# Kernel tuning notes

Hardware: AMD Instinct MI355X
Metric: run time of the kernel (lower is better)

## Reference

```python
import jax, jax.numpy as jnp
import numpy as np
from jax import lax

B, S, T, V, E, H = 32, 128, 64, 32000, 512, 512
STEPS = T - 1


def gru_cell(x, h, Wih, Whh, bih, bhh):
    # PyTorch GRU cell: gates ordered (r, z, n)
    gi = x @ Wih.T + bih            # [B, 3H]
    gh = h @ Whh.T + bhh            # [B, 3H]
    ir, iz, inn = jnp.split(gi, 3, axis=-1)
    hr, hz, hn = jnp.split(gh, 3, axis=-1)
    r = jax.nn.sigmoid(ir + hr)
    z = jax.nn.sigmoid(iz + hz)
    n = jnp.tanh(inn + r * hn)
    return (1.0 - z) * n + z * h


def setup_inputs() -> dict:
    key = jax.random.key(0)
    ks = jax.random.split(key, 16)
    w = lambda k, shape: (jax.random.normal(k, shape, dtype=jnp.float32) * 0.05)
    src = jax.random.randint(ks[0], (B, S), 1, V)
    src_lengths = jax.random.randint(ks[1], (B,), 1, S + 1)
    tgt = jax.random.randint(ks[2], (B, T), 1, V)
    return {
        'src': src, 'src_lengths': src_lengths, 'tgt': tgt,
        # encoder
        'emb_enc': w(ks[3], (V, E)).at[0].set(0.0),   # padding_idx=0
        'Wih_e': w(ks[4], (3 * H, E)),
        'Whh_e': w(ks[5], (3 * H, H)),
        'bih_e': jnp.zeros((3 * H,), jnp.float32),
        'bhh_e': jnp.zeros((3 * H,), jnp.float32),
        # decoder
        'emb_dec': w(ks[6], (V, E)).at[0].set(0.0),
        'Wih_d': w(ks[7], (3 * H, E + H)),
        'Whh_d': w(ks[8], (3 * H, H)),
        'bih_d': jnp.zeros((3 * H,), jnp.float32),
        'bhh_d': jnp.zeros((3 * H,), jnp.float32),
        'Wc': w(ks[9], (H, 2 * H)),
        'bc': jnp.zeros((H,), jnp.float32),
        'Wo': w(ks[10], (V, H)),
        'bo': jnp.zeros((V,), jnp.float32),
    }


def _forward(src, src_lengths, tgt, emb_enc, Wih_e, Whh_e, bih_e, bhh_e,
             emb_dec, Wih_d, Whh_d, bih_d, bhh_d, Wc, bc, Wo, bo):
    # ---- encoder (packed-sequence semantics: state frozen / outputs zero past length) ----
    x = emb_enc[src]                                   # [B, S, E]
    xs = jnp.swapaxes(x, 0, 1)                         # [S, B, E]
    valid = jnp.arange(S)[:, None] < src_lengths[None, :]  # [S, B]
    h0 = jnp.zeros((src.shape[0], H), x.dtype)

    def enc_step(h, inp):
        xt, vt = inp
        hn = gru_cell(xt, h, Wih_e, Whh_e, bih_e, bhh_e)
        h = jnp.where(vt[:, None], hn, h)
        out = jnp.where(vt[:, None], hn, 0.0)
        return h, out

    h_enc, enc_outs = lax.scan(enc_step, h0, (xs, valid))
    enc_outs = jnp.swapaxes(enc_outs, 0, 1)            # [B, S, H]
    mask = jnp.arange(S)[None, :] < src_lengths[:, None]  # [B, S]

    # ---- decoder loop (teacher forcing ratio 1.0 -> input = tgt[:, t]) ----
    tokens = jnp.swapaxes(tgt[:, :STEPS], 0, 1)        # [STEPS, B]

    def dec_step(h, tok):
        e = emb_dec[tok]                               # [B, E]
        query = h                                      # hidden[-1], 1 layer
        scores = jnp.einsum('bsh,bh->bs', enc_outs, query)
        scores = jnp.where(mask, scores, -jnp.inf)
        aw = jax.nn.softmax(scores, axis=1)            # [B, S]
        ctx = jnp.einsum('bs,bsh->bh', aw, enc_outs)   # [B, H]
        rnn_in = jnp.concatenate([e, ctx], axis=-1)    # [B, E+H]
        hn = gru_cell(rnn_in, h, Wih_d, Whh_d, bih_d, bhh_d)
        cc = jnp.tanh(jnp.concatenate([hn, ctx], axis=-1) @ Wc.T + bc)
        logits = cc @ Wo.T + bo                        # [B, V]
        return hn, (logits, aw)

    _, (logits, attns) = lax.scan(dec_step, h_enc, tokens)
    logits = jnp.swapaxes(logits, 0, 1)                # [B, STEPS, V]
    attns = jnp.swapaxes(attns, 0, 1)                  # [B, STEPS, S]
    return logits, attns


def reference(src, src_lengths, tgt, emb_enc, Wih_e, Whh_e, bih_e, bhh_e,
              emb_dec, Wih_d, Whh_d, bih_d, bhh_d, Wc, bc, Wo, bo):
    return _forward(src, src_lengths, tgt, emb_enc, Wih_e, Whh_e, bih_e, bhh_e,
                    emb_dec, Wih_d, Whh_d, bih_d, bhh_d, Wc, bc, Wo, bo)
```

## Files before the change

### kernel.cpp

```cpp
#include <hip/hip_runtime.h>
#include <hip/hip_fp16.h>
#include <cmath>

#define B_ 32
#define S_ 128
#define T_ 64
#define STEPS_ 63
#define V_ 32000
#define E_ 512
#define H_ 512

typedef __attribute__((ext_vector_type(4))) float f32x4;
typedef __attribute__((ext_vector_type(8))) short bf16x8;
typedef __attribute__((ext_vector_type(2))) _Float16 f16x2;

__device__ inline short f2bf(float x) {
  unsigned u = __builtin_bit_cast(unsigned, x);
  u = (u + 0x7fffu + ((u >> 16) & 1u)) >> 16;
  return (short)u;
}
__device__ inline float bf2f(short h) {
  unsigned u = ((unsigned)(unsigned short)h) << 16;
  return __builtin_bit_cast(float, u);
}
__device__ inline float fdot2(__half2 a, __half2 b, float c) {
#if __has_builtin(__builtin_amdgcn_fdot2)
  return __builtin_amdgcn_fdot2(__builtin_bit_cast(f16x2, a),
                                __builtin_bit_cast(f16x2, b), c, false);
#else
  float2 af = __half22float2(a), bf = __half22float2(b);
  return c + af.x * bf.x + af.y * bf.y;
#endif
}
__device__ inline __half2 bc2(unsigned v) { return __builtin_bit_cast(__half2, v); }
__device__ inline float sigm(float x) { return 1.f / (1.f + expf(-x)); }

__global__ __launch_bounds__(256) void k_pack_w3(
    const float* __restrict__ W, int ldw, int col0, __half* __restrict__ W3) {
  int idx = blockIdx.x * 256 + threadIdx.x;
  int up = idx & 255, g = (idx >> 8) % 3, kq = idx / 768;
  const float* r0 = W + (long)(g * 512 + 2 * up) * ldw + col0 + 4 * kq;
  const float* r1 = r0 + ldw;
  __half h[8];
  h[0] = __float2half(r0[0]); h[1] = __float2half(r0[1]);
  h[2] = __float2half(r1[0]); h[3] = __float2half(r1[1]);
  h[4] = __float2half(r0[2]); h[5] = __float2half(r0[3]);
  h[6] = __float2half(r1[2]); h[7] = __float2half(r1[3]);
  *(uint4*)(W3 + (long)idx * 8) = *(uint4*)h;
}

__global__ __launch_bounds__(256) void k_mfma_gemm(
    const float* __restrict__ A, const float* __restrict__ emb,
    const int* __restrict__ tok, int amode,
    const float* __restrict__ Bmat, long ldb,
    const float* __restrict__ bias,
    void* __restrict__ outp, long sb, long st,
    int M, int N, int K, int outmode, int passes) {
  __shared__ short Ah[128 * 40];
  __shared__ short Al[128 * 40];
  __shared__ short Bh[128 * 40];
  __shared__ short Bl[128 * 40];
  int t = threadIdx.x;
  int n0 = blockIdx.x * 128, m0 = blockIdx.y * 128;
  int ar = t >> 2, ac = (t & 3) * 8;

  const float* arow0;
  const float* arow1;
  {
    int m = m0 + ar;       int mc = m < M ? m : M - 1;
    int m2 = m0 + ar + 64; int mc2 = m2 < M ? m2 : M - 1;
    if (amode == 0) {
      arow0 = A + (long)mc * K;
      arow1 = A + (long)mc2 * K;
    } else {
      int b = mc & 31, q = mc >> 5;
      int tk = (amode == 1) ? tok[b * S_ + q] : tok[b * T_ + q];
      arow0 = emb + (long)tk * K;
      b = mc2 & 31; q = mc2 >> 5;
      tk = (amode == 1) ? tok[b * S_ + q] : tok[b * T_ + q];
      arow1 = emb + (long)tk * K;
    }
  }
  const float* brow0 = Bmat + (long)(n0 + ar) * ldb;
  const float* brow1 = Bmat + (long)(n0 + ar + 64) * ldb;

  int lane = t & 63, wave = t >> 6;
  int wm = (wave >> 1) * 64, wn = (wave & 1) * 64;
  int lr = lane & 15, lk = lane >> 4;
  f32x4 acc[4][4] = {};

  for (int k0 = 0; k0 < K; k0 += 32) {
    auto stage = [&](const float* rowp, short* Dh, short* Dl, int r) {
      float4 x0 = *(const float4*)(rowp + k0 + ac);
      float4 x1 = *(const float4*)(rowp + k0 + ac + 4);
      float xs[8] = {x0.x, x0.y, x0.z, x0.w, x1.x, x1.y, x1.z, x1.w};
      bf16x8 hi, lo;
#pragma unroll
      for (int i = 0; i < 8; ++i) {
        short h = f2bf(xs[i]);
        hi[i] = h;
        lo[i] = f2bf(xs[i] - bf2f(h));
      }
      *(bf16x8*)&Dh[r * 40 + ac] = hi;
      if (passes > 1) *(bf16x8*)&Dl[r * 40 + ac] = lo;
    };
    stage(arow0, Ah, Al, ar);
    stage(arow1, Ah, Al, ar + 64);
    stage(brow0, Bh, Bl, ar);
    stage(brow1, Bh, Bl, ar + 64);
    __syncthreads();

    bf16x8 a_h[4], b_h[4];
#pragma unroll
    for (int i = 0; i < 4; ++i) {
      a_h[i] = *(const bf16x8*)&Ah[(wm + i * 16 + lr) * 40 + lk * 8];
      b_h[i] = *(const bf16x8*)&Bh[(wn + i * 16 + lr) * 40 + lk * 8];
    }
    if (passes > 1) {
      bf16x8 a_l[4], b_l[4];
#pragma unroll
      for (int i = 0; i < 4; ++i) {
        a_l[i] = *(const bf16x8*)&Al[(wm + i * 16 + lr) * 40 + lk * 8];
        b_l[i] = *(const bf16x8*)&Bl[(wn + i * 16 + lr) * 40 + lk * 8];
      }
#pragma unroll
      for (int i = 0; i < 4; ++i)
#pragma unroll
        for (int j = 0; j < 4; ++j) {
          acc[i][j] = __builtin_amdgcn_mfma_f32_16x16x32_bf16(a_l[i], b_h[j], acc[i][j], 0, 0, 0);
          acc[i][j] = __builtin_amdgcn_mfma_f32_16x16x32_bf16(a_h[i], b_l[j], acc[i][j], 0, 0, 0);
        }
    }
#pragma unroll
    for (int i = 0; i < 4; ++i)
#pragma unroll
      for (int j = 0; j < 4; ++j)
        acc[i][j] = __builtin_amdgcn_mfma_f32_16x16x32_bf16(a_h[i], b_h[j], acc[i][j], 0, 0, 0);
    __syncthreads();
  }

#pragma unroll
  for (int i = 0; i < 4; ++i) {
#pragma unroll
    for (int r = 0; r < 4; ++r) {
      int m = m0 + wm + i * 16 + lk * 4 + r;
      if (m >= M) continue;
      long base = (long)(m & 31) * sb + (long)(m >> 5) * st;
#pragma unroll
      for (int j = 0; j < 4; ++j) {
        int n = n0 + wn + j * 16 + lr;
        float v = acc[i][j][r] + bias[n];
        if (outmode == 2) ((__half*)outp)[base + n] = __float2half(v);
        else ((float*)outp)[base + n] = (outmode == 1) ? tanhf(v) : v;
      }
    }
  }
}

__global__ __launch_bounds__(1024) void k_enc_all(
    const float* __restrict__ gi_all,
    const __half* __restrict__ W3,
    const float* __restrict__ bhh, const int* __restrict__ lens,
    float* __restrict__ h_out,
    __half* __restrict__ EO16,
    float* __restrict__ EO32) {
  __shared__ __align__(8) __half2 hs16[256];
  __shared__ float pGh[1536];
  __shared__ float gis[1536];
  int b = blockIdx.x, t = threadIdx.x;
  int len = lens[b];
  float br0 = 0, br1 = 0, bz0 = 0, bz1 = 0, bn0 = 0, bn1 = 0, hold0 = 0, hold1 = 0;
  if (t < 256) {
    br0 = bhh[2 * t]; br1 = bhh[2 * t + 1];
    bz0 = bhh[512 + 2 * t]; bz1 = bhh[512 + 2 * t + 1];
    bn0 = bhh[1024 + 2 * t]; bn1 = bhh[1024 + 2 * t + 1];
    hs16[t] = __float22half2_rn(make_float2(0.f, 0.f));
  }
  __syncthreads();

  for (int s = 0; s < S_; ++s) {
    if (s == len) break;
    if (t >= 256) {
      int c = t - 256, g = c >> 8, up = c & 255;
      const __half* wb = W3 + (long)(g * 256 + up) * 8;
      float a0 = 0.f, a1 = 0.f;
#pragma unroll 8
      for (int kq = 0; kq < 128; ++kq) {
        uint4 w8 = *(const uint4*)(wb + (long)kq * 6144);
        __half2 x01 = hs16[2 * kq], x23 = hs16[2 * kq + 1];
        a0 = fdot2(x01, bc2(w8.x), a0); a1 = fdot2(x01, bc2(w8.y), a1);
        a0 = fdot2(x23, bc2(w8.z), a0); a1 = fdot2(x23, bc2(w8.w), a1);
      }
      pGh[g * 512 + 2 * up] = a0;
      pGh[g * 512 + 2 * up + 1] = a1;
    } else {
      const float* gi = gi_all + ((long)s * 32 + b) * 1536;
      int i0 = t * 6;
#pragma unroll
      for (int i = 0; i < 6; ++i) gis[i0 + i] = gi[i0 + i];
    }
    __syncthreads();
    if (t < 256) {
      int u0 = 2 * t;
      float r0 = sigm(gis[u0] + pGh[u0] + br0);
      float r1 = sigm(gis[u0 + 1] + pGh[u0 + 1] + br1);
      float z0 = sigm(gis[512 + u0] + pGh[512 + u0] + bz0);
      float z1 = sigm(gis[512 + u0 + 1] + pGh[512 + u0 + 1] + bz1);
      float n0 = tanhf(gis[1024 + u0] + r0 * (pGh[1024 + u0] + bn0));
      float n1 = tanhf(gis[1024 + u0 + 1] + r1 * (pGh[1024 + u0 + 1] + bn1));
      hold0 = (1.f - z0) * n0 + z0 * hold0;
      hold1 = (1.f - z1) * n1 + z1 * hold1;
      __half2 h2 = __float22half2_rn(make_float2(hold0, hold1));
      hs16[t] = h2;
      long row = (long)b * 128 + s;
      *(__half2*)(EO16 + row * 512 + u0) = h2;
      *(float2*)(EO32 + row * 512 + u0) = make_float2(hold0, hold1);
    }
    __syncthreads();
  }
  if (t < 256) *(float2*)(h_out + b * 512 + 2 * t) = make_float2(hold0, hold1);
}

__global__ __launch_bounds__(1024) void k_dec_all(
    const float* __restrict__ gie,
    const __half* __restrict__ EO16g,
    const __half* __restrict__ W3,
    const __half* __restrict__ GV,
    const float* __restrict__ bhh, const int* __restrict__ lens,
    const float* __restrict__ h_init,
    float* __restrict__ hctx,
    float* __restrict__ attns) {
  __shared__ __align__(16) __half2 EOs[32768];
  __shared__ __align__(8) __half2 hs16[256];
  __shared__ float pGh[1536];
  __shared__ float pGc[1536];
  __shared__ float gis[1536];
  __shared__ float sc[128];
  int b = blockIdx.x, t = threadIdx.x;
  int lane = t & 63, wave = t >> 6;
  int len = lens[b];
  float br0 = 0, br1 = 0, bz0 = 0, bz1 = 0, bn0 = 0, bn1 = 0, hold0 = 0, hold1 = 0;
  if (t < 256) {
    br0 = bhh[2 * t]; br1 = bhh[2 * t + 1];
    bz0 = bhh[512 + 2 * t]; bz1 = bhh[512 + 2 * t + 1];
    bn0 = bhh[1024 + 2 * t]; bn1 = bhh[1024 + 2 * t + 1];
    float2 h2 = *(const float2*)(h_init + b * 512 + 2 * t);
    hold0 = h2.x; hold1 = h2.y;
    hs16[t] = __float22half2_rn(h2);
  }
  {
    const uint4* src = (const uint4*)(EO16g + (long)b * 128 * 512);
    uint4* dst = (uint4*)EOs;
    for (int i = t; i < 8192; i += 1024) dst[i] = src[i];
  }
  __syncthreads();
  const __half2* GVb = (const __half2*)GV + (long)b * 128 * 768;

  for (int step = 0; step < STEPS_; ++step) {
    long row = (long)step * 32 + b;
    if (t < 768) {
      int g = t >> 8, up = t & 255;
      const __half* wb = W3 + (long)(g * 256 + up) * 8;
      float a0 = 0.f, a1 = 0.f;
#pragma unroll 8
      for (int kq = 0; kq < 128; ++kq) {
        uint4 w8 = *(const uint4*)(wb + (long)kq * 6144);
        __half2 x01 = hs16[2 * kq], x23 = hs16[2 * kq + 1];
        a0 = fdot2(x01, bc2(w8.x), a0); a1 = fdot2(x01, bc2(w8.y), a1);
        a0 = fdot2(x23, bc2(w8.z), a0); a1 = fdot2(x23, bc2(w8.w), a1);
      }
      pGh[g * 512 + 2 * up] = a0;
      pGh[g * 512 + 2 * up + 1] = a1;
    } else {
      int w = wave - 12;
      uint4 hv = ((const uint4*)hs16)[lane];
      __half2 h0 = bc2(hv.x), h1 = bc2(hv.y), h2 = bc2(hv.z), h3 = bc2(hv.w);
#pragma unroll 4
      for (int si = 0; si < 32; ++si) {
        int s = w * 32 + si;
        uint4 ev = ((const uint4*)&EOs[s * 256])[lane];
        float p = 0.f;
        p = fdot2(bc2(ev.x), h0, p);
        p = fdot2(bc2(ev.y), h1, p);
        p = fdot2(bc2(ev.z), h2, p);
        p = fdot2(bc2(ev.w), h3, p);
#pragma unroll
        for (int off = 32; off > 0; off >>= 1) p += __shfl_down(p, off, 64);
        if (lane == 0) sc[s] = p;
      }
    }
    __syncthreads();
    if (t < 64) {
      float p0 = sc[lane], p1 = sc[64 + lane];
      bool v0 = lane < len, v1 = 64 + lane < len;
      float m = fmaxf(v0 ? p0 : -INFINITY, v1 ? p1 : -INFINITY);
#pragma unroll
      for (int off = 32; off > 0; off >>= 1) m = fmaxf(m, __shfl_xor(m, off, 64));
      float e0 = v0 ? expf(p0 - m) : 0.f;
      float e1 = v1 ? expf(p1 - m) : 0.f;
      float S = e0 + e1;
#pragma unroll
      for (int off = 32; off > 0; off >>= 1) S += __shfl_xor(S, off, 64);
      float aw0 = e0 / S, aw1 = e1 / S;
      sc[lane] = aw0;
      sc[64 + lane] = aw1;
      float* ap = attns + ((long)b * STEPS_ + step) * 128;
      ap[lane] = aw0;
      ap[64 + lane] = aw1;
    } else if (t < 448) {
      int i0 = (t - 64) * 4;
      *(float4*)(gis + i0) = *(const float4*)(gie + row * 1536 + i0);
    }
    __syncthreads();
    if (t < 768) {
      float ax = 0.f, ay = 0.f;
      for (int s = 0; s < 128; ++s) {
        if (s == len) break;
        float aw = sc[s];
        float2 g2 = __half22float2(GVb[(long)s * 768 + t]);
        ax += aw * g2.x;
        ay += aw * g2.y;
      }
      pGc[2 * t] = ax;
      pGc[2 * t + 1] = ay;
    } else {
      int c = t - 768;
      float ax = 0.f, ay = 0.f;
      for (int s = 0; s < 128; ++s) {
        if (s == len) break;
        float aw = sc[s];
        float2 e2 = __half22float2(EOs[s * 256 + c]);
        ax += aw * e2.x;
        ay += aw * e2.y;
      }
      *(float2*)(hctx + row * 1024 + 512 + 2 * c) = make_float2(ax, ay);
    }
    __syncthreads();
    if (t < 256) {
      int u0 = 2 * t;
      float r0 = sigm(gis[u0] + pGc[u0] + pGh[u0] + br0);
      float r1 = sigm(gis[u0 + 1] + pGc[u0 + 1] + pGh[u0 + 1] + br1);
      float z0 = sigm(gis[512 + u0] + pGc[512 + u0] + pGh[512 + u0] + bz0);
      float z1 = sigm(gis[512 + u0 + 1] + pGc[512 + u0 + 1] + pGh[512 + u0 + 1] + bz1);
      float n0 = tanhf(gis[1024 + u0] + pGc[1024 + u0] + r0 * (pGh[1024 + u0] + bn0));
      float n1 = tanhf(gis[1024 + u0 + 1] + pGc[1024 + u0 + 1] + r1 * (pGh[1024 + u0 + 1] + bn1));
      hold0 = (1.f - z0) * n0 + z0 * hold0;
      hold1 = (1.f - z1) * n1 + z1 * hold1;
      hs16[t] = __float22half2_rn(make_float2(hold0, hold1));
      *(float2*)(hctx + row * 1024 + u0) = make_float2(hold0, hold1);
    }
    __syncthreads();
  }
}

extern "C" void kernel_launch(void* const* d_in, const int* in_sizes, int n_in,
                              void* d_out, int out_size, void* d_ws, size_t ws_size,
                              hipStream_t stream) {
  (void)in_sizes; (void)n_in; (void)out_size; (void)ws_size;
  const int*   src   = (const int*)d_in[0];
  const int*   lens  = (const int*)d_in[1];
  const int*   tgt   = (const int*)d_in[2];
  const float* emb_e = (const float*)d_in[3];
  const float* Wih_e = (const float*)d_in[4];
  const float* Whh_e = (const float*)d_in[5];
  const float* bih_e = (const float*)d_in[6];
  const float* bhh_e = (const float*)d_in[7];
  const float* emb_d = (const float*)d_in[8];
  const float* Wih_d = (const float*)d_in[9];
  const float* Whh_d = (const float*)d_in[10];
  const float* bih_d = (const float*)d_in[11];
  const float* bhh_d = (const float*)d_in[12];
  const float* Wc    = (const float*)d_in[13];
  const float* bc    = (const float*)d_in[14];
  const float* Wo    = (const float*)d_in[15];
  const float* bo    = (const float*)d_in[16];

  float* logits = (float*)d_out;
  float* attns  = (float*)d_out + (long)B_ * STEPS_ * V_;

  float* w = (float*)d_ws;
  __half* W3e  = (__half*)w;
  __half* W3d  = (__half*)(w + 393216);
  float*  zb   = w + 786432;
  float*  GIe  = w + 788480;
  float*  GId  = GIe + 6291456;
  __half* EO16 = (__half*)(GId + 3145728);
  float*  EO32 = GId + 3145728 + 1048576;
  float*  h0   = EO32 + 2097152;
  __half* GV    = (__half*)GIe;
  float*  hctx  = GIe + 3145728;
  float*  ccall = GIe + 5242880;

  hipMemsetAsync(EO16, 0, 2097152 * sizeof(__half), stream);
  hipMemsetAsync(EO32, 0, 2097152 * sizeof(float), stream);
  hipMemsetAsync(zb, 0, 1536 * sizeof(float), stream);

  k_pack_w3<<<384, 256, 0, stream>>>(Whh_e, 512, 0, W3e);
  k_pack_w3<<<384, 256, 0, stream>>>(Whh_d, 512, 0, W3d);

  k_mfma_gemm<<<dim3(1536 / 128, 4096 / 128), 256, 0, stream>>>(
      nullptr, emb_e, src, 1, Wih_e, 512, bih_e, GIe, 1536L, 32L * 1536L,
      4096, 1536, 512, 0, 1);
  k_mfma_gemm<<<dim3(1536 / 128, (2016 + 127) / 128), 256, 0, stream>>>(
      nullptr, emb_d, tgt, 2, Wih_d, 1024, bih_d, GId, 1536L, 32L * 1536L,
      2016, 1536, 512, 0, 1);

  k_enc_all<<<32, 1024, 0, stream>>>(GIe, W3e, bhh_e, lens, h0, EO16, EO32);

  k_mfma_gemm<<<dim3(1536 / 128, 4096 / 128), 256, 0, stream>>>(
      EO32, nullptr, nullptr, 0, Wih_d + 512, 1024, zb, GV, 1536L, 49152L,
      4096, 1536, 512, 2, 1);

  k_dec_all<<<32, 1024, 0, stream>>>(GId, EO16, W3d, GV, bhh_d, lens, h0,
                                     hctx, attns);

  k_mfma_gemm<<<dim3(512 / 128, (2016 + 127) / 128), 256, 0, stream>>>(
      hctx, nullptr, nullptr, 0, Wc, 1024, bc, ccall, 512L, 16384L,
      2016, 512, 1024, 1, 1);

  k_mfma_gemm<<<dim3(V_ / 128, (2016 + 127) / 128), 256, 0, stream>>>(
      ccall, nullptr, nullptr, 0, Wo, 512, bo, logits,
      (long)STEPS_ * V_, (long)V_, 2016, 32000, 512, 0, 1);
}
```

Measured before the change: 2.976 ms.

## Split encoder GRU recurrence across two cooperating blocks per batch with flag sync

Each batch row's encoder recurrence is now handled by two blocks, each computing half the hidden units and half of each K reduction per thread. The halves exchange fp16 hidden state through a global buffer and release/acquire flags every timestep. The aim is to halve the per-step serial matvec latency and use more CUs. In exchange it adds cross-block spin-wait latency each step and relies on all 64 blocks being co-resident.

Result: slower. 3.162 ms (+6.3%).

```diff
diff --git a/kernel.cpp b/kernel.cpp
--- a/kernel.cpp
+++ b/kernel.cpp
@@ -163,62 +163,103 @@
     const float* __restrict__ bhh, const int* __restrict__ lens,
     float* __restrict__ h_out,
     __half* __restrict__ EO16,
-    float* __restrict__ EO32) {
+    float* __restrict__ EO32,
+    unsigned* __restrict__ hbuf,
+    int* __restrict__ flags) {
   __shared__ __align__(8) __half2 hs16[256];
-  __shared__ float pGh[1536];
-  __shared__ float gis[1536];
-  int b = blockIdx.x, t = threadIdx.x;
+  __shared__ float pGh[768];
+  __shared__ float gis[768];
+  int blk = blockIdx.x, t = threadIdx.x;
+  int b = blk & 31, half = blk >> 5;
   int len = lens[b];
-  float br0 = 0, br1 = 0, bz0 = 0, bz1 = 0, bn0 = 0, bn1 = 0, hold0 = 0, hold1 = 0;
-  if (t < 256) {
-    br0 = bhh[2 * t]; br1 = bhh[2 * t + 1];
-    bz0 = bhh[512 + 2 * t]; bz1 = bhh[512 + 2 * t + 1];
-    bn0 = bhh[1024 + 2 * t]; bn1 = bhh[1024 + 2 * t + 1];
-    hs16[t] = __float22half2_rn(make_float2(0.f, 0.f));
-  }
+  int u0g = half * 256;
+  int* flagOwn = flags + b * 2 + half;
+  int* flagP   = flags + b * 2 + (1 - half);
+  unsigned* hbOwn = hbuf + (b * 2 + half) * 128;
+  unsigned* hbP   = hbuf + (b * 2 + (1 - half)) * 128;
+  float br0 = 0, br1 = 0, bz0 = 0, bz1 = 0, bn0 = 0, bn1 = 0;
+  float hold0 = 0.f, hold1 = 0.f;
+  if (t < 128) {
+    int u = u0g + 2 * t;
+    br0 = bhh[u]; br1 = bhh[u + 1];
+    bz0 = bhh[512 + u]; bz1 = bhh[512 + u + 1];
+    bn0 = bhh[1024 + u]; bn1 = bhh[1024 + u + 1];
+  }
+  if (t < 256) hs16[t] = __float22half2_rn(make_float2(0.f, 0.f));
   __syncthreads();
+
+  int c = t - 256;
+  int g = c >> 8, rem = c & 255;
+  int up_loc = rem >> 1, kh2 = rem & 1;
+  int up = half * 128 + up_loc;
+  const __half* wb = W3 + (long)(kh2 * 64) * 6144 + (long)(g * 256 + up) * 8;
 
   for (int s = 0; s < S_; ++s) {
     if (s == len) break;
+    if (s > 0) {
+      if (t == 0) {
+        while (__hip_atomic_load(flagP, __ATOMIC_ACQUIRE, __HIP_MEMORY_SCOPE_AGENT) < s)
+          __builtin_amdgcn_s_sleep(1);
+      }
+      __syncthreads();
+      if (t < 128) {
+        unsigned v = __hip_atomic_load(hbP + t, __ATOMIC_RELAXED, __HIP_MEMORY_SCOPE_AGENT);
+        hs16[(1 - half) * 128 + t] = bc2(v);
+      }
+    }
+    __syncthreads();
     if (t >= 256) {
-      int c = t - 256, g = c >> 8, up = c & 255;
-      const __half* wb = W3 + (long)(g * 256 + up) * 8;
       float a0 = 0.f, a1 = 0.f;
 #pragma unroll 8
-      for (int kq = 0; kq < 128; ++kq) {
-        uint4 w8 = *(const uint4*)(wb + (long)kq * 6144);
+      for (int kq2 = 0; kq2 < 64; ++kq2) {
+        uint4 w8 = *(const uint4*)(wb + (long)kq2 * 6144);
+        int kq = kh2 * 64 + kq2;
         __half2 x01 = hs16[2 * kq], x23 = hs16[2 * kq + 1];
         a0 = fdot2(x01, bc2(w8.x), a0); a1 = fdot2(x01, bc2(w8.y), a1);
         a0 = fdot2(x23, bc2(w8.z), a0); a1 = fdot2(x23, bc2(w8.w), a1);
       }
-      pGh[g * 512 + 2 * up] = a0;
-      pGh[g * 512 + 2 * up + 1] = a1;
-    } else {
+      a0 += __shfl_xor(a0, 1, 64);
+      a1 += __shfl_xor(a1, 1, 64);
+      if (kh2 == 0) {
+        pGh[g * 256 + 2 * up_loc] = a0;
+        pGh[g * 256 + 2 * up_loc + 1] = a1;
+      }
+    } else if (t >= 128) {
       const float* gi = gi_all + ((long)s * 32 + b) * 1536;
-      int i0 = t * 6;
-#pragma unroll
-      for (int i = 0; i < 6; ++i) gis[i0 + i] = gi[i0 + i];
-    }
-    __syncthreads();
-    if (t < 256) {
-      int u0 = 2 * t;
-      float r0 = sigm(gis[u0] + pGh[u0] + br0);
-      float r1 = sigm(gis[u0 + 1] + pGh[u0 + 1] + br1);
-      float z0 = sigm(gis[512 + u0] + pGh[512 + u0] + bz0);
-      float z1 = sigm(gis[512 + u0 + 1] + pGh[512 + u0 + 1] + bz1);
-      float n0 = tanhf(gis[1024 + u0] + r0 * (pGh[1024 + u0] + bn0));
-      float n1 = tanhf(gis[1024 + u0 + 1] + r1 * (pGh[1024 + u0 + 1] + bn1));
+      int i = t - 128;
+      gis[2 * i] = gi[u0g + 2 * i];
+      gis[2 * i + 1] = gi[u0g + 2 * i + 1];
+      gis[256 + 2 * i] = gi[512 + u0g + 2 * i];
+      gis[256 + 2 * i + 1] = gi[512 + u0g + 2 * i + 1];
+      gis[512 + 2 * i] = gi[1024 + u0g + 2 * i];
+      gis[512 + 2 * i + 1] = gi[1024 + u0g + 2 * i + 1];
+    }
+    __syncthreads();
+    if (t < 128) {
+      int l0 = 2 * t;
+      float r0 = sigm(gis[l0] + pGh[l0] + br0);
+      float r1 = sigm(gis[l0 + 1] + pGh[l0 + 1] + br1);
+      float z0 = sigm(gis[256 + l0] + pGh[256 + l0] + bz0);
+      float z1 = sigm(gis[256 + l0 + 1] + pGh[256 + l0 + 1] + bz1);
+      float n0 = tanhf(gis[512 + l0] + r0 * (pGh[512 + l0] + bn0));
+      float n1 = tanhf(gis[512 + l0 + 1] + r1 * (pGh[512 + l0 + 1] + bn1));
       hold0 = (1.f - z0) * n0 + z0 * hold0;
       hold1 = (1.f - z1) * n1 + z1 * hold1;
       __half2 h2 = __float22half2_rn(make_float2(hold0, hold1));
-      hs16[t] = h2;
+      hs16[half * 128 + t] = h2;
       long row = (long)b * 128 + s;
-      *(__half2*)(EO16 + row * 512 + u0) = h2;
-      *(float2*)(EO32 + row * 512 + u0) = make_float2(hold0, hold1);
-    }
-    __syncthreads();
-  }
-  if (t < 256) *(float2*)(h_out + b * 512 + 2 * t) = make_float2(hold0, hold1);
+      *(__half2*)(EO16 + row * 512 + u0g + l0) = h2;
+      *(float2*)(EO32 + row * 512 + u0g + l0) = make_float2(hold0, hold1);
+      __hip_atomic_store(hbOwn + t, __builtin_bit_cast(unsigned, h2),
+                         __ATOMIC_RELAXED, __HIP_MEMORY_SCOPE_AGENT);
+    }
+    __syncthreads();
+    if (t == 0) {
+      __threadfence();
+      __hip_atomic_store(flagOwn, s + 1, __ATOMIC_RELEASE, __HIP_MEMORY_SCOPE_AGENT);
+    }
+  }
+  if (t < 128) *(float2*)(h_out + b * 512 + u0g + 2 * t) = make_float2(hold0, hold1);
 }
 
 __global__ __launch_bounds__(1024) void k_dec_all(
@@ -387,6 +428,8 @@
   __half* EO16 = (__half*)(GId + 3145728);
   float*  EO32 = GId + 3145728 + 1048576;
   float*  h0   = EO32 + 2097152;
+  unsigned* hbuf  = (unsigned*)(h0 + 16384);
+  int*      flags = (int*)(hbuf + 8192);
   __half* GV    = (__half*)GIe;
   float*  hctx  = GIe + 3145728;
   float*  ccall = GIe + 5242880;
@@ -394,6 +437,7 @@
   hipMemsetAsync(EO16, 0, 2097152 * sizeof(__half), stream);
   hipMemsetAsync(EO32, 0, 2097152 * sizeof(float), stream);
   hipMemsetAsync(zb, 0, 1536 * sizeof(float), stream);
+  hipMemsetAsync(flags, 0, 64 * sizeof(int), stream);
 
   k_pack_w3<<<384, 256, 0, stream>>>(Whh_e, 512, 0, W3e);
   k_pack_w3<<<384, 256, 0, stream>>>(Whh_d, 512, 0, W3d);
@@ -405,7 +449,8 @@
       nullptr, emb_d, tgt, 2, Wih_d, 1024, bih_d, GId, 1536L, 32L * 1536L,
       2016, 1536, 512, 0, 1);
 
-  k_enc_all<<<32, 1024, 0, stream>>>(GIe, W3e, bhh_e, lens, h0, EO16, EO32);
+  k_enc_all<<<64, 1024, 0, stream>>>(GIe, W3e, bhh_e, lens, h0, EO16, EO32,
+                                     hbuf, flags);
 
   k_mfma_gemm<<<dim3(1536 / 128, 4096 / 128), 256, 0, stream>>>(
       EO32, nullptr, nullptr, 0, Wih_d + 512, 1024, zb, GV, 1536L, 49152L,
```

## Split encoder GRU across blocks by hidden unit with global flag synchronization

Applied to the files above, without the earlier changes.

The encoder recurrence used to run one block per batch element, and each block streamed the full Whh matrix every timestep. It now launches 16 blocks, each owning 32 hidden units for all 32 batch rows. Each thread keeps its weight row in a repacked per-unit layout. Hidden states are exchanged through a double-buffered global array with per-block acquire/release flags, and padding is handled by freezing state past each row's length. This spreads the weight traffic across blocks and reuses each weight load across batch rows. In exchange it adds a cross-block spin barrier every step, it no longer stops early for short sequences, and the 16 blocks must all be resident at once for the barrier to make progress.

Result: slower. 4.859 ms (+63.3%).

```diff
diff --git a/kernel.cpp b/kernel.cpp
--- a/kernel.cpp
+++ b/kernel.cpp
@@ -34,6 +34,17 @@
 }
 __device__ inline __half2 bc2(unsigned v) { return __builtin_bit_cast(__half2, v); }
 __device__ inline float sigm(float x) { return 1.f / (1.f + expf(-x)); }
+
+__global__ __launch_bounds__(256) void k_pack_w5(
+    const float* __restrict__ W, int ldw, int col0, uint4* __restrict__ W5) {
+  int idx = blockIdx.x * 256 + threadIdx.x;
+  int g = idx % 3, kq4 = (idx / 3) & 63, u = idx / 192;
+  const float* r = W + (long)(g * 512 + u) * ldw + col0 + 8 * kq4;
+  __half h[8];
+#pragma unroll
+  for (int j = 0; j < 8; ++j) h[j] = __float2half(r[j]);
+  W5[idx] = *(uint4*)h;
+}
 
 __global__ __launch_bounds__(256) void k_pack_w3(
     const float* __restrict__ W, int ldw, int col0, __half* __restrict__ W3) {
@@ -159,66 +170,98 @@
 
 __global__ __launch_bounds__(1024) void k_enc_all(
     const float* __restrict__ gi_all,
-    const __half* __restrict__ W3,
+    const uint4* __restrict__ W5,
     const float* __restrict__ bhh, const int* __restrict__ lens,
     float* __restrict__ h_out,
     __half* __restrict__ EO16,
-    float* __restrict__ EO32) {
-  __shared__ __align__(8) __half2 hs16[256];
-  __shared__ float pGh[1536];
-  __shared__ float gis[1536];
-  int b = blockIdx.x, t = threadIdx.x;
-  int len = lens[b];
-  float br0 = 0, br1 = 0, bz0 = 0, bz1 = 0, bn0 = 0, bn1 = 0, hold0 = 0, hold1 = 0;
-  if (t < 256) {
-    br0 = bhh[2 * t]; br1 = bhh[2 * t + 1];
-    bz0 = bhh[512 + 2 * t]; bz1 = bhh[512 + 2 * t + 1];
-    bn0 = bhh[1024 + 2 * t]; bn1 = bhh[1024 + 2 * t + 1];
-    hs16[t] = __float22half2_rn(make_float2(0.f, 0.f));
-  }
-  __syncthreads();
+    float* __restrict__ EO32,
+    unsigned* __restrict__ hball,
+    int* __restrict__ flags) {
+  __shared__ __half2 h_lds[32][257];
+  __shared__ float gis[3][32][33];
+  __shared__ int lenS[32];
+  int blk = blockIdx.x, t = threadIdx.x;
+  int u_loc = t >> 5, b = t & 31;
+  int u0 = blk * 32, u = u0 + u_loc;
+  float bhr = bhh[u], bhz = bhh[512 + u], bhn = bhh[1024 + u];
+  float hcur = 0.f;
+  const uint4* wp = W5 + (long)u * 192;
+  if (t < 32) lenS[t] = lens[t];
+  int len_b = lens[b];
 
   for (int s = 0; s < S_; ++s) {
-    if (s == len) break;
-    if (t >= 256) {
-      int c = t - 256, g = c >> 8, up = c & 255;
-      const __half* wb = W3 + (long)(g * 256 + up) * 8;
-      float a0 = 0.f, a1 = 0.f;
+    int par = s & 1;
+    if (s > 0) {
+      if (t < 16 && t != blk) {
+        while (__hip_atomic_load(flags + t, __ATOMIC_ACQUIRE, __HIP_MEMORY_SCOPE_AGENT) < s)
+          __builtin_amdgcn_s_sleep(1);
+      }
+      __syncthreads();
+    }
+    {
+      const unsigned* hb = hball + par * 8192;
+#pragma unroll
+      for (int j = 0; j < 8; ++j) {
+        int idx = j * 1024 + t;
+        unsigned v = __hip_atomic_load(hb + idx, __ATOMIC_RELAXED, __HIP_MEMORY_SCOPE_AGENT);
+        h_lds[idx >> 8][idx & 255] = bc2(v);
+      }
+#pragma unroll
+      for (int j = 0; j < 3; ++j) {
+        int idx = j * 1024 + t;
+        int bb = (idx >> 5) & 31, e = idx & 31;
+        gis[j][bb][e] = gi_all[((long)s * 32 + bb) * 1536 + j * 512 + u0 + e];
+      }
+    }
+    __syncthreads();
+    float ar = 0.f, az = 0.f, an = 0.f;
 #pragma unroll 8
-      for (int kq = 0; kq < 128; ++kq) {
-        uint4 w8 = *(const uint4*)(wb + (long)kq * 6144);
-        __half2 x01 = hs16[2 * kq], x23 = hs16[2 * kq + 1];
-        a0 = fdot2(x01, bc2(w8.x), a0); a1 = fdot2(x01, bc2(w8.y), a1);
-        a0 = fdot2(x23, bc2(w8.z), a0); a1 = fdot2(x23, bc2(w8.w), a1);
-      }
-      pGh[g * 512 + 2 * up] = a0;
-      pGh[g * 512 + 2 * up + 1] = a1;
-    } else {
-      const float* gi = gi_all + ((long)s * 32 + b) * 1536;
-      int i0 = t * 6;
-#pragma unroll
-      for (int i = 0; i < 6; ++i) gis[i0 + i] = gi[i0 + i];
-    }
-    __syncthreads();
-    if (t < 256) {
-      int u0 = 2 * t;
-      float r0 = sigm(gis[u0] + pGh[u0] + br0);
-      float r1 = sigm(gis[u0 + 1] + pGh[u0 + 1] + br1);
-      float z0 = sigm(gis[512 + u0] + pGh[512 + u0] + bz0);
-      float z1 = sigm(gis[512 + u0 + 1] + pGh[512 + u0 + 1] + bz1);
-      float n0 = tanhf(gis[1024 + u0] + r0 * (pGh[1024 + u0] + bn0));
-      float n1 = tanhf(gis[1024 + u0 + 1] + r1 * (pGh[1024 + u0 + 1] + bn1));
-      hold0 = (1.f - z0) * n0 + z0 * hold0;
-      hold1 = (1.f - z1) * n1 + z1 * hold1;
-      __half2 h2 = __float22half2_rn(make_float2(hold0, hold1));
-      hs16[t] = h2;
-      long row = (long)b * 128 + s;
-      *(__half2*)(EO16 + row * 512 + u0) = h2;
-      *(float2*)(EO32 + row * 512 + u0) = make_float2(hold0, hold1);
-    }
-    __syncthreads();
-  }
-  if (t < 256) *(float2*)(h_out + b * 512 + 2 * t) = make_float2(hold0, hold1);
+    for (int kq4 = 0; kq4 < 64; ++kq4) {
+      __half2 h0 = h_lds[b][4 * kq4 + 0];
+      __half2 h1 = h_lds[b][4 * kq4 + 1];
+      __half2 h2 = h_lds[b][4 * kq4 + 2];
+      __half2 h3 = h_lds[b][4 * kq4 + 3];
+      uint4 wr = wp[kq4 * 3 + 0];
+      uint4 wz = wp[kq4 * 3 + 1];
+      uint4 wn = wp[kq4 * 3 + 2];
+      ar = fdot2(h0, bc2(wr.x), ar); ar = fdot2(h1, bc2(wr.y), ar);
+      ar = fdot2(h2, bc2(wr.z), ar); ar = fdot2(h3, bc2(wr.w), ar);
+      az = fdot2(h0, bc2(wz.x), az); az = fdot2(h1, bc2(wz.y), az);
+      az = fdot2(h2, bc2(wz.z), az); az = fdot2(h3, bc2(wz.w), az);
+      an = fdot2(h0, bc2(wn.x), an); an = fdot2(h1, bc2(wn.y), an);
+      an = fdot2(h2, bc2(wn.z), an); an = fdot2(h3, bc2(wn.w), an);
+    }
+    __syncthreads();
+    {
+      bool valid = s < len_b;
+      float r = sigm(gis[0][b][u_loc] + ar + bhr);
+      float z = sigm(gis[1][b][u_loc] + az + bhz);
+      float n = tanhf(gis[2][b][u_loc] + r * (an + bhn));
+      float hn = (1.f - z) * n + z * hcur;
+      if (valid) hcur = hn;
+      ((__half*)&h_lds[b][0])[u] = __float2half(hcur);
+    }
+    __syncthreads();
+    if (t < 512) {
+      int bb = t >> 4, p = t & 15;
+      __half2 v2 = h_lds[bb][u0 / 2 + p];
+      __hip_atomic_store(hball + (par ^ 1) * 8192 + bb * 256 + u0 / 2 + p,
+                         __builtin_bit_cast(unsigned, v2),
+                         __ATOMIC_RELAXED, __HIP_MEMORY_SCOPE_AGENT);
+      if (s < lenS[bb]) {
+        long row = (long)bb * 128 + s;
+        *(__half2*)(EO16 + row * 512 + u0 + 2 * p) = v2;
+        float2 f2 = __half22float2(v2);
+        *(float2*)(EO32 + row * 512 + u0 + 2 * p) = f2;
+      }
+    }
+    __syncthreads();
+    if (t == 0) {
+      __threadfence();
+      __hip_atomic_store(flags + blk, s + 1, __ATOMIC_RELEASE, __HIP_MEMORY_SCOPE_AGENT);
+    }
+  }
+  h_out[b * 512 + u] = hcur;
 }
 
 __global__ __launch_bounds__(1024) void k_dec_all(
@@ -379,7 +422,7 @@
   float* attns  = (float*)d_out + (long)B_ * STEPS_ * V_;
 
   float* w = (float*)d_ws;
-  __half* W3e  = (__half*)w;
+  uint4*  W5e  = (uint4*)w;
   __half* W3d  = (__half*)(w + 393216);
   float*  zb   = w + 786432;
   float*  GIe  = w + 788480;
@@ -387,6 +430,8 @@
   __half* EO16 = (__half*)(GId + 3145728);
   float*  EO32 = GId + 3145728 + 1048576;
   float*  h0   = EO32 + 2097152;
+  unsigned* hball = (unsigned*)(h0 + 16384);
+  int*      flags = (int*)(hball + 16384);
   __half* GV    = (__half*)GIe;
   float*  hctx  = GIe + 3145728;
   float*  ccall = GIe + 5242880;
@@ -394,8 +439,10 @@
   hipMemsetAsync(EO16, 0, 2097152 * sizeof(__half), stream);
   hipMemsetAsync(EO32, 0, 2097152 * sizeof(float), stream);
   hipMemsetAsync(zb, 0, 1536 * sizeof(float), stream);
-
-  k_pack_w3<<<384, 256, 0, stream>>>(Whh_e, 512, 0, W3e);
+  hipMemsetAsync(hball, 0, 16384 * sizeof(unsigned), stream);
+  hipMemsetAsync(flags, 0, 16 * sizeof(int), stream);
+
+  k_pack_w5<<<384, 256, 0, stream>>>(Whh_e, 512, 0, W5e);
   k_pack_w3<<<384, 256, 0, stream>>>(Whh_d, 512, 0, W3d);
 
   k_mfma_gemm<<<dim3(1536 / 128, 4096 / 128), 256, 0, stream>>>(
@@ -405,7 +452,8 @@
       nullptr, emb_d, tgt, 2, Wih_d, 1024, bih_d, GId, 1536L, 32L * 1536L,
       2016, 1536, 512, 0, 1);
 
-  k_enc_all<<<32, 1024, 0, stream>>>(GIe, W3e, bhh_e, lens, h0, EO16, EO32);
+  k_enc_all<<<16, 1024, 0, stream>>>(GIe, W5e, bhh_e, lens, h0, EO16, EO32,
+                                     hball, flags);
 
   k_mfma_gemm<<<dim3(1536 / 128, 4096 / 128), 256, 0, stream>>>(
       EO32, nullptr, nullptr, 0, Wih_d + 512, 1024, zb, GV, 1536L, 49152L,
```

## Drop fp32 encoder outputs, read fp16 in GEMM, overlap decoder matvec with softmax

Applied to the files above, without the earlier changes.

The encoder no longer writes a second fp32 copy of its outputs. The follow-on GEMM gains an A-operand mode that reads the fp16 encoder outputs directly, which also removes one memset and one large buffer. In the decoder loop, the hidden-state matvec is split into two halves so the second half runs alongside the softmax and the gate-input load across the barrier. The fp16 source changes GEMM precision slightly, though the bf16 staging already rounds it, and the split work may add register pressure.

After: 3.167 ms. +6.4%, slower.

```diff
diff --git a/kernel.cpp b/kernel.cpp
--- a/kernel.cpp
+++ b/kernel.cpp
@@ -72,6 +72,9 @@
     if (amode == 0) {
       arow0 = A + (long)mc * K;
       arow1 = A + (long)mc2 * K;
+    } else if (amode == 3) {
+      arow0 = (const float*)((const __half*)A + (long)mc * K);
+      arow1 = (const float*)((const __half*)A + (long)mc2 * K);
     } else {
       int b = mc & 31, q = mc >> 5;
       int tk = (amode == 1) ? tok[b * S_ + q] : tok[b * T_ + q];
@@ -90,10 +93,7 @@
   f32x4 acc[4][4] = {};
 
   for (int k0 = 0; k0 < K; k0 += 32) {
-    auto stage = [&](const float* rowp, short* Dh, short* Dl, int r) {
-      float4 x0 = *(const float4*)(rowp + k0 + ac);
-      float4 x1 = *(const float4*)(rowp + k0 + ac + 4);
-      float xs[8] = {x0.x, x0.y, x0.z, x0.w, x1.x, x1.y, x1.z, x1.w};
+    auto pack = [&](const float xs[8], short* Dh, short* Dl, int r) {
       bf16x8 hi, lo;
 #pragma unroll
       for (int i = 0; i < 8; ++i) {
@@ -104,10 +104,33 @@
       *(bf16x8*)&Dh[r * 40 + ac] = hi;
       if (passes > 1) *(bf16x8*)&Dl[r * 40 + ac] = lo;
     };
-    stage(arow0, Ah, Al, ar);
-    stage(arow1, Ah, Al, ar + 64);
-    stage(brow0, Bh, Bl, ar);
-    stage(brow1, Bh, Bl, ar + 64);
+    auto stageA = [&](const float* rowp, int r) {
+      float xs[8];
+      if (amode == 3) {
+        uint4 hv = *(const uint4*)((const __half*)rowp + k0 + ac);
+        const __half* hp = (const __half*)&hv;
+#pragma unroll
+        for (int i = 0; i < 8; ++i) xs[i] = __half2float(hp[i]);
+      } else {
+        float4 x0 = *(const float4*)(rowp + k0 + ac);
+        float4 x1 = *(const float4*)(rowp + k0 + ac + 4);
+        xs[0] = x0.x; xs[1] = x0.y; xs[2] = x0.z; xs[3] = x0.w;
+        xs[4] = x1.x; xs[5] = x1.y; xs[6] = x1.z; xs[7] = x1.w;
+      }
+      pack(xs, Ah, Al, r);
+    };
+    auto stageB = [&](const float* rowp, int r) {
+      float xs[8];
+      float4 x0 = *(const float4*)(rowp + k0);
+      float4 x1 = *(const float4*)(rowp + k0 + 4);
+      xs[0] = x0.x; xs[1] = x0.y; xs[2] = x0.z; xs[3] = x0.w;
+      xs[4] = x1.x; xs[5] = x1.y; xs[6] = x1.z; xs[7] = x1.w;
+      pack(xs, Bh, Bl, r);
+    };
+    stageA(arow0, ar);
+    stageA(arow1, ar + 64);
+    stageB(brow0 + ac, ar);
+    stageB(brow1 + ac, ar + 64);
     __syncthreads();
 
     bf16x8 a_h[4], b_h[4];
@@ -162,8 +185,7 @@
     const __half* __restrict__ W3,
     const float* __restrict__ bhh, const int* __restrict__ lens,
     float* __restrict__ h_out,
-    __half* __restrict__ EO16,
-    float* __restrict__ EO32) {
+    __half* __restrict__ EO16) {
   __shared__ __align__(8) __half2 hs16[256];
   __shared__ float pGh[1536];
   __shared__ float gis[1536];
@@ -212,9 +234,7 @@
       hold1 = (1.f - z1) * n1 + z1 * hold1;
       __half2 h2 = __float22half2_rn(make_float2(hold0, hold1));
       hs16[t] = h2;
-      long row = (long)b * 128 + s;
-      *(__half2*)(EO16 + row * 512 + u0) = h2;
-      *(float2*)(EO32 + row * 512 + u0) = make_float2(hold0, hold1);
+      *(__half2*)(EO16 + ((long)b * 128 + s) * 512 + u0) = h2;
     }
     __syncthreads();
   }
@@ -258,19 +278,20 @@
 
   for (int step = 0; step < STEPS_; ++step) {
     long row = (long)step * 32 + b;
+    float a0 = 0.f, a1 = 0.f;
+    const __half* wb = nullptr;
     if (t < 768) {
       int g = t >> 8, up = t & 255;
-      const __half* wb = W3 + (long)(g * 256 + up) * 8;
-      float a0 = 0.f, a1 = 0.f;
+      wb = W3 + (long)(g * 256 + up) * 8;
+    }
+    if (t < 768) {
 #pragma unroll 8
-      for (int kq = 0; kq < 128; ++kq) {
+      for (int kq = 0; kq < 64; ++kq) {
         uint4 w8 = *(const uint4*)(wb + (long)kq * 6144);
         __half2 x01 = hs16[2 * kq], x23 = hs16[2 * kq + 1];
         a0 = fdot2(x01, bc2(w8.x), a0); a1 = fdot2(x01, bc2(w8.y), a1);
         a0 = fdot2(x23, bc2(w8.z), a0); a1 = fdot2(x23, bc2(w8.w), a1);
       }
-      pGh[g * 512 + 2 * up] = a0;
-      pGh[g * 512 + 2 * up + 1] = a1;
     } else {
       int w = wave - 12;
       uint4 hv = ((const uint4*)hs16)[lane];
@@ -290,9 +311,21 @@
       }
     }
     __syncthreads();
-    if (t < 64) {
-      float p0 = sc[lane], p1 = sc[64 + lane];
-      bool v0 = lane < len, v1 = 64 + lane < len;
+    if (t < 768) {
+#pragma unroll 8
+      for (int kq = 64; kq < 128; ++kq) {
+        uint4 w8 = *(const uint4*)(wb + (long)kq * 6144);
+        __half2 x01 = hs16[2 * kq], x23 = hs16[2 * kq + 1];
+        a0 = fdot2(x01, bc2(w8.x), a0); a1 = fdot2(x01, bc2(w8.y), a1);
+        a0 = fdot2(x23, bc2(w8.z), a0); a1 = fdot2(x23, bc2(w8.w), a1);
+      }
+      int g = t >> 8, up = t & 255;
+      pGh[g * 512 + 2 * up] = a0;
+      pGh[g * 512 + 2 * up + 1] = a1;
+    } else if (t < 832) {
+      int l = t - 768;
+      float p0 = sc[l], p1 = sc[64 + l];
+      bool v0 = l < len, v1 = 64 + l < len;
       float m = fmaxf(v0 ? p0 : -INFINITY, v1 ? p1 : -INFINITY);
 #pragma unroll
       for (int off = 32; off > 0; off >>= 1) m = fmaxf(m, __shfl_xor(m, off, 64));
@@ -302,14 +335,16 @@
 #pragma unroll
       for (int off = 32; off > 0; off >>= 1) S += __shfl_xor(S, off, 64);
       float aw0 = e0 / S, aw1 = e1 / S;
-      sc[lane] = aw0;
-      sc[64 + lane] = aw1;
+      sc[l] = aw0;
+      sc[64 + l] = aw1;
       float* ap = attns + ((long)b * STEPS_ + step) * 128;
-      ap[lane] = aw0;
-      ap[64 + lane] = aw1;
-    } else if (t < 448) {
-      int i0 = (t - 64) * 4;
-      *(float4*)(gis + i0) = *(const float4*)(gie + row * 1536 + i0);
+      ap[l] = aw0;
+      ap[64 + l] = aw1;
+    } else {
+      int i0 = (t - 832) * 8;
+      const float* gp = gie + row * 1536 + i0;
+      *(float4*)(gis + i0) = *(const float4*)(gp);
+      *(float4*)(gis + i0 + 4) = *(const float4*)(gp + 4);
     }
     __syncthreads();
     if (t < 768) {
@@ -385,14 +420,12 @@
   float*  GIe  = w + 788480;
   float*  GId  = GIe + 6291456;
   __half* EO16 = (__half*)(GId + 3145728);
-  float*  EO32 = GId + 3145728 + 1048576;
-  float*  h0   = EO32 + 2097152;
+  float*  h0   = GId + 3145728 + 1048576;
   __half* GV    = (__half*)GIe;
   float*  hctx  = GIe + 3145728;
   float*  ccall = GIe + 5242880;
 
   hipMemsetAsync(EO16, 0, 2097152 * sizeof(__half), stream);
-  hipMemsetAsync(EO32, 0, 2097152 * sizeof(float), stream);
   hipMemsetAsync(zb, 0, 1536 * sizeof(float), stream);
 
   k_pack_w3<<<384, 256, 0, stream>>>(Whh_e, 512, 0, W3e);
@@ -405,11 +438,11 @@
       nullptr, emb_d, tgt, 2, Wih_d, 1024, bih_d, GId, 1536L, 32L * 1536L,
       2016, 1536, 512, 0, 1);
 
-  k_enc_all<<<32, 1024, 0, stream>>>(GIe, W3e, bhh_e, lens, h0, EO16, EO32);
+  k_enc_all<<<32, 1024, 0, stream>>>(GIe, W3e, bhh_e, lens, h0, EO16);
 
   k_mfma_gemm<<<dim3(1536 / 128, 4096 / 128), 256, 0, stream>>>(
-      EO32, nullptr, nullptr, 0, Wih_d + 512, 1024, zb, GV, 1536L, 49152L,
-      4096, 1536, 512, 2, 1);
+      (const float*)EO16, nullptr, nullptr, 3, Wih_d + 512, 1024, zb, GV,
+      1536L, 49152L, 4096, 1536, 512, 2, 1);
 
   k_dec_all<<<32, 1024, 0, stream>>>(GId, EO16, W3d, GV, bhh_d, lens, h0,
                                      hctx, attns);
```
